# Kernel tuning notes

Hardware: AMD Instinct MI355X
Metric: run time of the kernel (lower is better)

## Reference

```python
import jax, jax.numpy as jnp
import numpy as np

B, S, D, H, E, K = 4, 1024, 1024, 4096, 8, 2


def setup_inputs() -> dict:
    key = jax.random.key(0)
    k1, k2, k3, k4 = jax.random.split(key, 4)
    x = jax.random.normal(k1, (B, S, D), dtype=jnp.float32)
    # expert params: two-layer MLP per expert, stacked along expert axis
    W1 = jax.random.normal(k2, (E, D, H), dtype=jnp.float32) * 0.02
    b1 = jnp.zeros((E, H), dtype=jnp.float32)
    W2 = jax.random.normal(k3, (E, H, D), dtype=jnp.float32) * 0.02
    b2 = jnp.zeros((E, D), dtype=jnp.float32)
    # hash-router assignments: k expert ids per token (stands in for HashRouter output)
    assign = jax.random.randint(k4, (B, S, K), 0, E, dtype=jnp.int64)
    return {"x": x, "W1": W1, "b1": b1, "W2": W2, "b2": b2, "assign": assign, "k": K}


def reference(x, W1, b1, W2, b2, assign, k):
    E_ = W1.shape[0]
    # mask[b,s,e] = 1 if expert e appears in assign[b,s,:] (matches (assign==idx).any(-1),
    # so a duplicated assignment contributes once, exactly like the torch loop)
    mask = (assign[..., None] == jnp.arange(E_)[None, None, None, :]).any(axis=-2)
    # run every token through every expert, then mask-combine (dense MoE reference)
    h = jax.nn.relu(jnp.einsum('bsd,edh->bseh', x, W1) + b1)      # [B,S,E,H]
    y = jnp.einsum('bseh,ehd->bsed', h, W2) + b2                  # [B,S,E,D]
    out = jnp.einsum('bsed,bse->bsd', y, mask.astype(x.dtype))
    return out / k
```

## Files before the change

kernel.cpp:

```cpp
#include <hip/hip_runtime.h>
#include <hip/hip_bf16.h>

#define DIM_D 1024
#define DIM_H 4096
#define NUM_E 8
#define NUM_TOK 4096
#define MAXROWS 8320

typedef __attribute__((ext_vector_type(8))) short short8;
typedef __attribute__((ext_vector_type(4))) float floatx4;

__device__ __forceinline__ unsigned short f2bf(float f) {
  union { float f; unsigned int u; } v; v.f = f;
  unsigned int r = v.u + 0x7fffu + ((v.u >> 16) & 1u);
  return (unsigned short)(r >> 16);
}

__device__ __forceinline__ void async_copy16(const void* g, void* l) {
  __builtin_amdgcn_global_load_lds(
      (__attribute__((address_space(1))) unsigned int*)(g),
      (__attribute__((address_space(3))) unsigned int*)(l), 16, 0, 0);
}

__global__ __launch_bounds__(256) void route_scan(
    const int* __restrict__ assign, int* __restrict__ counts,
    int* __restrict__ offsets, int* __restrict__ tok2row) {
  __shared__ int hist[256][NUM_E];
  __shared__ int base[NUM_E];
  const int tid = threadIdx.x;
  const int t0 = tid * 16;
#pragma unroll
  for (int e = 0; e < NUM_E; e++) hist[tid][e] = 0;
  const int4* ap = (const int4*)(assign + t0 * 2);
  for (int i = 0; i < 8; i++) {
    int4 v = ap[i];
    hist[tid][v.x]++; if (v.y != v.x) hist[tid][v.y]++;
    hist[tid][v.z]++; if (v.w != v.z) hist[tid][v.w]++;
  }
  __syncthreads();
  if (tid < NUM_E) {
    int acc = 0;
    for (int i = 0; i < 256; i++) { int v = hist[i][tid]; hist[i][tid] = acc; acc += v; }
    base[tid] = acc;
  }
  __syncthreads();
  if (tid == 0) {
    int acc = 0;
    for (int e = 0; e < NUM_E; e++) {
      int tot = base[e];
      counts[e] = tot; offsets[e] = acc; base[e] = acc; acc += tot;
    }
  }
  __syncthreads();
#pragma unroll
  for (int e = 0; e < NUM_E; e++) hist[tid][e] += base[e];
  for (int i = 0; i < 8; i++) {
    int4 v = ap[i];
    int t = t0 + 2 * i;
    int4 o;
    o.x = hist[tid][v.x]++;
    o.y = (v.y != v.x) ? hist[tid][v.y]++ : -1;
    o.z = hist[tid][v.z]++;
    o.w = (v.w != v.z) ? hist[tid][v.w]++ : -1;
    *(int4*)(tok2row + 2 * t) = o;
  }
}

__global__ void gather_x(const float* __restrict__ x, const int* __restrict__ tok2row,
                         unsigned short* __restrict__ Xg) {
  int t = blockIdx.x;
  int r0 = tok2row[2 * t], r1 = tok2row[2 * t + 1];
  const float4* xv = (const float4*)(x + (size_t)t * DIM_D);
  float4 v0 = xv[threadIdx.x * 2];
  float4 v1 = xv[threadIdx.x * 2 + 1];
  unsigned short h[8];
  h[0] = f2bf(v0.x); h[1] = f2bf(v0.y); h[2] = f2bf(v0.z); h[3] = f2bf(v0.w);
  h[4] = f2bf(v1.x); h[5] = f2bf(v1.y); h[6] = f2bf(v1.z); h[7] = f2bf(v1.w);
  uint4 pack = *(uint4*)h;
  *(uint4*)(Xg + (size_t)r0 * DIM_D + threadIdx.x * 8) = pack;
  if (r1 >= 0)
    *(uint4*)(Xg + (size_t)r1 * DIM_D + threadIdx.x * 8) = pack;
}

#define TPT 8
__global__ __launch_bounds__(256) void transpose_cvt64(
    const float* __restrict__ W1, const float* __restrict__ W2,
    unsigned short* __restrict__ W1t, unsigned short* __restrict__ W2t) {
  __shared__ float tile[2][64 * 64];
  const int tid = threadIdx.x;
  const int gbase = blockIdx.x * TPT;
  const int z = gbase >> 10;
  const int m0 = gbase & 1023;
  const int e = z >> 1, which = z & 1;
  const int R = which ? DIM_H : DIM_D;
  const int C = which ? DIM_D : DIM_H;
  const int nbx = C / 64;
  const float* in0 = (which ? W2 : W1) + (size_t)e * R * C;
  unsigned short* out0 = (which ? W2t : W1t) + (size_t)e * R * C;

  const int chunk = tid & 15, rb = tid >> 4;
  const int s = tid & 7, c0 = tid >> 3;
  const int by = m0 / nbx;
  const int bx0 = m0 % nbx;
  const float* ipbase = in0 + (size_t)(by * 64) * C + (size_t)bx0 * 64;

  float4 rA[4], rB[4];
#pragma unroll
  for (int p = 0; p < 4; p++)
    rA[p] = *(const float4*)(ipbase + (size_t)(rb + p * 16) * C + chunk * 4);

#pragma unroll
  for (int i = 0; i < TPT; i++) {
    float* buf = tile[i & 1];
#pragma unroll
    for (int p = 0; p < 4; p++) {
      int r = rb + p * 16;
      int slot = chunk ^ (r >> 3);
      *(float4*)&buf[r * 64 + slot * 4] = (i & 1) ? rB[p] : rA[p];
    }
    if (i + 1 < TPT) {
      const float* ip = ipbase + (size_t)(i + 1) * 64;
#pragma unroll
      for (int p = 0; p < 4; p++) {
        float4 v = *(const float4*)(ip + (size_t)(rb + p * 16) * C + chunk * 4);
        if (i & 1) rA[p] = v; else rB[p] = v;
      }
    }
    __syncthreads();
    unsigned short* op = out0 + (size_t)((bx0 + i) * 64) * R + by * 64;
#pragma unroll
    for (int ii = 0; ii < 2; ii++) {
      int c = c0 + ii * 32;
      int base = (((c >> 2) ^ s) * 4) + (c & 3);
      unsigned short h[8];
#pragma unroll
      for (int j = 0; j < 8; j++) h[j] = f2bf(buf[(8 * s + j) * 64 + base]);
      *(uint4*)(op + (size_t)c * R + 8 * s) = *(const uint4*)h;
    }
  }
}

template <int MODE, int KTOT>
__global__ __launch_bounds__(256) void moe_gemm(
    const unsigned short* __restrict__ Ain, const unsigned short* __restrict__ Bt,
    const float* __restrict__ bias, const int* __restrict__ counts,
    const int* __restrict__ offsets,
    unsigned short* __restrict__ Hout, float* __restrict__ Yout,
    int lda, int ldb, int N) {
  int e, half;
  if (MODE == 0) { e = blockIdx.z; half = 0; }
  else           { e = blockIdx.z >> 1; half = blockIdx.z & 1; }
  const int cnt = counts[e];
  int mt_, nt_;
  if (MODE == 0) {
    int l = blockIdx.x;
    int xcd = l & 7, sIdx = l >> 3;
    nt_ = xcd * 4 + (sIdx & 3);
    mt_ = sIdx >> 2;
  } else {
    int l = blockIdx.x;
    nt_ = l & 7;
    mt_ = l >> 3;
  }
  const int m0 = mt_ * 128;
  if (m0 >= cnt) return;
  const int n0 = nt_ * 128;
  const int rowbase = offsets[e];
  const unsigned short* A = Ain + (size_t)half * KTOT;

  __shared__ unsigned short sh[2 * 128 * 64];
  unsigned short* As = sh;
  unsigned short* Bs = sh + 128 * 64;

  const int tid = threadIdx.x;
  const int w = tid >> 6;
  const int lane = tid & 63;
  const int l15 = lane & 15, l4 = lane >> 4;
  const int wm = w >> 1, wn = w & 1;
  const int lrow = lane >> 3, lslot = lane & 7;
  const int lchunk = lslot ^ lrow;

  const unsigned short* gA[4]; const unsigned short* gB[4];
  void* dA[4]; void* dB[4];
  const unsigned short* Bbase = Bt + (size_t)e * N * ldb + (size_t)half * KTOT;
#pragma unroll
  for (int p = 0; p < 4; p++) {
    int rw = p * 32 + w * 8;
    gA[p] = A + (size_t)(rowbase + m0 + rw + lrow) * lda + lchunk * 8;
    gB[p] = Bbase + (size_t)(n0 + rw + lrow) * ldb + lchunk * 8;
    dA[p] = (char*)As + rw * 128;
    dB[p] = (char*)Bs + rw * 128;
  }

  floatx4 acc[4][4];
#pragma unroll
  for (int i = 0; i < 4; i++)
#pragma unroll
    for (int j = 0; j < 4; j++) acc[i][j] = (floatx4){0.f, 0.f, 0.f, 0.f};

  int arow[4], brow[4], sl[2];
  sl[0] = ((l4 + 0) ^ (l15 & 7)) * 8;
  sl[1] = ((l4 + 4) ^ (l15 & 7)) * 8;
#pragma unroll
  for (int mt = 0; mt < 4; mt++) arow[mt] = (wm * 64 + mt * 16 + l15) * 64;
#pragma unroll
  for (int nt = 0; nt < 4; nt++) brow[nt] = (wn * 64 + nt * 16 + l15) * 64;

  for (int k0 = 0; k0 < KTOT; k0 += 64) {
    __syncthreads();
#pragma unroll
    for (int p = 0; p < 4; p++) async_copy16(gA[p], dA[p]);
#pragma unroll
    for (int p = 0; p < 4; p++) async_copy16(gB[p], dB[p]);
#pragma unroll
    for (int p = 0; p < 4; p++) { gA[p] += 64; gB[p] += 64; }
    __syncthreads();
#pragma unroll
    for (int s = 0; s < 2; s++) {
      short8 a[4], b[4];
#pragma unroll
      for (int mt = 0; mt < 4; mt++) a[mt] = *(const short8*)(As + arow[mt] + sl[s]);
#pragma unroll
      for (int nt = 0; nt < 4; nt++) b[nt] = *(const short8*)(Bs + brow[nt] + sl[s]);
#pragma unroll
      for (int mt = 0; mt < 4; mt++)
#pragma unroll
        for (int nt = 0; nt < 4; nt++)
          acc[mt][nt] = __builtin_amdgcn_mfma_f32_16x16x32_bf16(a[mt], b[nt], acc[mt][nt], 0, 0, 0);
    }
  }

  __syncthreads();
  float* sbuf = (float*)sh + w * 1088;
  const bool addb = (MODE == 0) || (half == 0);
  const float* be = bias + (size_t)e * N + n0 + wn * 64;
  float* yplane = (MODE == 1) ? (Yout + (size_t)half * MAXROWS * N) : nullptr;
#pragma unroll
  for (int mt = 0; mt < 4; mt++) {
#pragma unroll
    for (int nt = 0; nt < 4; nt++) {
      float bv = addb ? be[nt * 16 + l15] : 0.f;
#pragma unroll
      for (int r = 0; r < 4; r++) {
        float v = acc[mt][nt][r] + bv;
        if (MODE == 0) v = fmaxf(v, 0.f);
        sbuf[(l4 * 4 + r) * 68 + nt * 16 + l15] = v;
      }
    }
    __asm__ __volatile__("s_waitcnt lgkmcnt(0)" ::: "memory");
#pragma unroll
    for (int pass = 0; pass < 4; pass++) {
      int row = pass * 4 + l4;
      int col4 = l15 * 4;
      int gm = m0 + wm * 64 + mt * 16 + row;
      float4 v = *(const float4*)&sbuf[row * 68 + col4];
      if (gm < cnt) {
        size_t off = (size_t)(rowbase + gm) * N + n0 + wn * 64 + col4;
        if (MODE == 0) {
          ushort4 h;
          h.x = f2bf(v.x); h.y = f2bf(v.y); h.z = f2bf(v.z); h.w = f2bf(v.w);
          *(ushort4*)(Hout + off) = h;
        } else {
          *(float4*)(yplane + off) = v;
        }
      }
    }
    __asm__ __volatile__("s_waitcnt lgkmcnt(0)" ::: "memory");
  }
}

__global__ void combine_k(const float* __restrict__ Yg, const int* __restrict__ tok2row,
                          const int* __restrict__ kptr, float* __restrict__ out) {
  int t = blockIdx.x;
  int r0 = tok2row[2 * t], r1 = tok2row[2 * t + 1];
  float invk = 1.0f / (float)kptr[0];
  int d = threadIdx.x * 4;
  const size_t plane = (size_t)MAXROWS * DIM_D;
  float4 v = *(const float4*)(Yg + (size_t)r0 * DIM_D + d);
  float4 u = *(const float4*)(Yg + plane + (size_t)r0 * DIM_D + d);
  v.x += u.x; v.y += u.y; v.z += u.z; v.w += u.w;
  if (r1 >= 0) {
    float4 a = *(const float4*)(Yg + (size_t)r1 * DIM_D + d);
    float4 b = *(const float4*)(Yg + plane + (size_t)r1 * DIM_D + d);
    v.x += a.x + b.x; v.y += a.y + b.y; v.z += a.z + b.z; v.w += a.w + b.w;
  }
  float4 o; o.x = v.x * invk; o.y = v.y * invk; o.z = v.z * invk; o.w = v.w * invk;
  *(float4*)(out + (size_t)t * DIM_D + d) = o;
}


extern "C" void kernel_launch(void* const* d_in, const int* in_sizes, int n_in,
                              void* d_out, int out_size, void* d_ws, size_t ws_size,
                              hipStream_t stream) {
  const float* x = (const float*)d_in[0];
  const float* W1 = (const float*)d_in[1];
  const float* b1 = (const float*)d_in[2];
  const float* W2 = (const float*)d_in[3];
  const float* b2 = (const float*)d_in[4];
  const int* assign = (const int*)d_in[5];
  const int* kptr = (const int*)d_in[6];
  float* out = (float*)d_out;

  char* p = (char*)d_ws;
  int* counts = (int*)p; p += 256;
  int* offsets = (int*)p; p += 256;
  int* tok2row = (int*)p; p += NUM_TOK * 2 * 4;
  unsigned short* W1t = (unsigned short*)p; p += (size_t)NUM_E * DIM_D * DIM_H * 2;
  unsigned short* Xg = (unsigned short*)p; p += (size_t)MAXROWS * DIM_D * 2;
  unsigned short* Hg = (unsigned short*)p; p += (size_t)MAXROWS * DIM_H * 2;
  unsigned short* W2t = (unsigned short*)p; p += (size_t)NUM_E * DIM_D * DIM_H * 2;
  float* Yg = (float*)W1t;

  route_scan<<<1, 256, 0, stream>>>(assign, counts, offsets, tok2row);
  gather_x<<<NUM_TOK, 128, 0, stream>>>(x, tok2row, Xg);

  transpose_cvt64<<<16384 / TPT, 256, 0, stream>>>(W1, W2, W1t, W2t);

  moe_gemm<0, DIM_D><<<dim3(1024, 1, NUM_E), 256, 0, stream>>>(
      Xg, W1t, b1, counts, offsets, Hg, nullptr, DIM_D, DIM_D, DIM_H);
  moe_gemm<1, DIM_H / 2><<<dim3(256, 1, NUM_E * 2), 256, 0, stream>>>(
      Hg, W2t, b2, counts, offsets, nullptr, Yg, DIM_H, DIM_H, DIM_D);

  combine_k<<<NUM_TOK, 256, 0, stream>>>(Yg, tok2row, kptr, out);
}
```

Baseline: 549.9 us.

## Build compact expert tile table to launch only live GEMM tiles

The routing kernel now emits a table of (expert, row-offset) tiles, and both expert GEMMs index that table through blockIdx.y. This replaces the fixed per-expert grids in which many blocks exited early. It also drops the XCD-aware tile swizzle in the first GEMM, which could hurt L2 reuse. The weight transpose goes from a double-buffered shared tile to a single buffer with an extra barrier, which halves LDS use but adds synchronisation. The grid is hardcoded to 72 tiles while the table can hold up to MAXTILES, which risks skipping tiles if the routing is more skewed.

```diff
diff --git a/kernel.cpp b/kernel.cpp
--- a/kernel.cpp
+++ b/kernel.cpp
@@ -6,6 +6,7 @@
 #define NUM_E 8
 #define NUM_TOK 4096
 #define MAXROWS 8320
+#define MAXTILES 80
 
 typedef __attribute__((ext_vector_type(8))) short short8;
 typedef __attribute__((ext_vector_type(4))) float floatx4;
@@ -24,7 +25,8 @@
 
 __global__ __launch_bounds__(256) void route_scan(
     const int* __restrict__ assign, int* __restrict__ counts,
-    int* __restrict__ offsets, int* __restrict__ tok2row) {
+    int* __restrict__ offsets, int* __restrict__ tok2row,
+    int* __restrict__ tiletab) {
   __shared__ int hist[256][NUM_E];
   __shared__ int base[NUM_E];
   const int tid = threadIdx.x;
@@ -45,11 +47,18 @@
   }
   __syncthreads();
   if (tid == 0) {
-    int acc = 0;
+    int acc = 0, ntile = 0;
     for (int e = 0; e < NUM_E; e++) {
       int tot = base[e];
       counts[e] = tot; offsets[e] = acc; base[e] = acc; acc += tot;
-    }
+      int nb = (tot + 127) >> 7;
+      for (int mb = 0; mb < nb; mb++) {
+        tiletab[1 + 2 * ntile] = e;
+        tiletab[2 + 2 * ntile] = mb << 7;
+        ntile++;
+      }
+    }
+    tiletab[0] = ntile;
   }
   __syncthreads();
 #pragma unroll
@@ -86,7 +95,7 @@
 __global__ __launch_bounds__(256) void transpose_cvt64(
     const float* __restrict__ W1, const float* __restrict__ W2,
     unsigned short* __restrict__ W1t, unsigned short* __restrict__ W2t) {
-  __shared__ float tile[2][64 * 64];
+  __shared__ float tile[64 * 64];
   const int tid = threadIdx.x;
   const int gbase = blockIdx.x * TPT;
   const int z = gbase >> 10;
@@ -104,27 +113,23 @@
   const int bx0 = m0 % nbx;
   const float* ipbase = in0 + (size_t)(by * 64) * C + (size_t)bx0 * 64;
 
-  float4 rA[4], rB[4];
+  float4 cur[4], nxt[4];
 #pragma unroll
   for (int p = 0; p < 4; p++)
-    rA[p] = *(const float4*)(ipbase + (size_t)(rb + p * 16) * C + chunk * 4);
-
-#pragma unroll
+    cur[p] = *(const float4*)(ipbase + (size_t)(rb + p * 16) * C + chunk * 4);
+
   for (int i = 0; i < TPT; i++) {
-    float* buf = tile[i & 1];
 #pragma unroll
     for (int p = 0; p < 4; p++) {
       int r = rb + p * 16;
       int slot = chunk ^ (r >> 3);
-      *(float4*)&buf[r * 64 + slot * 4] = (i & 1) ? rB[p] : rA[p];
+      *(float4*)&tile[r * 64 + slot * 4] = cur[p];
     }
     if (i + 1 < TPT) {
       const float* ip = ipbase + (size_t)(i + 1) * 64;
 #pragma unroll
-      for (int p = 0; p < 4; p++) {
-        float4 v = *(const float4*)(ip + (size_t)(rb + p * 16) * C + chunk * 4);
-        if (i & 1) rA[p] = v; else rB[p] = v;
-      }
+      for (int p = 0; p < 4; p++)
+        nxt[p] = *(const float4*)(ip + (size_t)(rb + p * 16) * C + chunk * 4);
     }
     __syncthreads();
     unsigned short* op = out0 + (size_t)((bx0 + i) * 64) * R + by * 64;
@@ -134,8 +139,13 @@
       int base = (((c >> 2) ^ s) * 4) + (c & 3);
       unsigned short h[8];
 #pragma unroll
-      for (int j = 0; j < 8; j++) h[j] = f2bf(buf[(8 * s + j) * 64 + base]);
+      for (int j = 0; j < 8; j++) h[j] = f2bf(tile[(8 * s + j) * 64 + base]);
       *(uint4*)(op + (size_t)c * R + 8 * s) = *(const uint4*)h;
+    }
+    if (i + 1 < TPT) {
+      __syncthreads();
+#pragma unroll
+      for (int p = 0; p < 4; p++) cur[p] = nxt[p];
     }
   }
 }
@@ -144,27 +154,16 @@
 __global__ __launch_bounds__(256) void moe_gemm(
     const unsigned short* __restrict__ Ain, const unsigned short* __restrict__ Bt,
     const float* __restrict__ bias, const int* __restrict__ counts,
-    const int* __restrict__ offsets,
+    const int* __restrict__ offsets, const int* __restrict__ tiletab,
     unsigned short* __restrict__ Hout, float* __restrict__ Yout,
     int lda, int ldb, int N) {
-  int e, half;
-  if (MODE == 0) { e = blockIdx.z; half = 0; }
-  else           { e = blockIdx.z >> 1; half = blockIdx.z & 1; }
+  const int tile = blockIdx.y;
+  if (tile >= tiletab[0]) return;
+  const int e = tiletab[1 + 2 * tile];
+  const int m0 = tiletab[2 + 2 * tile];
+  const int half = (MODE == 0) ? 0 : blockIdx.z;
   const int cnt = counts[e];
-  int mt_, nt_;
-  if (MODE == 0) {
-    int l = blockIdx.x;
-    int xcd = l & 7, sIdx = l >> 3;
-    nt_ = xcd * 4 + (sIdx & 3);
-    mt_ = sIdx >> 2;
-  } else {
-    int l = blockIdx.x;
-    nt_ = l & 7;
-    mt_ = l >> 3;
-  }
-  const int m0 = mt_ * 128;
-  if (m0 >= cnt) return;
-  const int n0 = nt_ * 128;
+  const int n0 = blockIdx.x * 128;
   const int rowbase = offsets[e];
   const unsigned short* A = Ain + (size_t)half * KTOT;
 
@@ -304,6 +303,7 @@
   char* p = (char*)d_ws;
   int* counts = (int*)p; p += 256;
   int* offsets = (int*)p; p += 256;
+  int* tiletab = (int*)p; p += 1024;
   int* tok2row = (int*)p; p += NUM_TOK * 2 * 4;
   unsigned short* W1t = (unsigned short*)p; p += (size_t)NUM_E * DIM_D * DIM_H * 2;
   unsigned short* Xg = (unsigned short*)p; p += (size_t)MAXROWS * DIM_D * 2;
@@ -311,15 +311,15 @@
   unsigned short* W2t = (unsigned short*)p; p += (size_t)NUM_E * DIM_D * DIM_H * 2;
   float* Yg = (float*)W1t;
 
-  route_scan<<<1, 256, 0, stream>>>(assign, counts, offsets, tok2row);
+  route_scan<<<1, 256, 0, stream>>>(assign, counts, offsets, tok2row, tiletab);
   gather_x<<<NUM_TOK, 128, 0, stream>>>(x, tok2row, Xg);
 
   transpose_cvt64<<<16384 / TPT, 256, 0, stream>>>(W1, W2, W1t, W2t);
 
-  moe_gemm<0, DIM_D><<<dim3(1024, 1, NUM_E), 256, 0, stream>>>(
-      Xg, W1t, b1, counts, offsets, Hg, nullptr, DIM_D, DIM_D, DIM_H);
-  moe_gemm<1, DIM_H / 2><<<dim3(256, 1, NUM_E * 2), 256, 0, stream>>>(
-      Hg, W2t, b2, counts, offsets, nullptr, Yg, DIM_H, DIM_H, DIM_D);
+  moe_gemm<0, DIM_D><<<dim3(32, 72, 1), 256, 0, stream>>>(
+      Xg, W1t, b1, counts, offsets, tiletab, Hg, nullptr, DIM_D, DIM_D, DIM_H);
+  moe_gemm<1, DIM_H / 2><<<dim3(8, 72, 2), 256, 0, stream>>>(
+      Hg, W2t, b2, counts, offsets, tiletab, nullptr, Yg, DIM_H, DIM_H, DIM_D);
 
   combine_k<<<NUM_TOK, 256, 0, stream>>>(Yg, tok2row, kptr, out);
 }
```

Result: slower. 645.1 us (+17.3%).
